# Kernel tuning notes

Hardware: AMD Instinct MI355X
Metric: run time of the kernel (lower is better)

## Reference

```python
import jax, jax.numpy as jnp
import numpy as np

B = 65536
STATE_DIM = 96
ACTION_DIM = 32
IN_FEATURES = STATE_DIM + ACTION_DIM  # 128
HIDDEN = 256
NUM_HEADS = 200
OUT_FEATURES = 1


def setup_inputs() -> dict:
    key = jax.random.key(0)
    ks = jax.random.split(key, 9)
    state = jax.random.normal(ks[0], (B, STATE_DIM), dtype=jnp.float32)
    action = jax.random.normal(ks[1], (B, ACTION_DIM), dtype=jnp.float32)
    alphas = jax.random.uniform(ks[2], (NUM_HEADS,), dtype=jnp.float32)
    W1 = jax.random.normal(ks[3], (HIDDEN, IN_FEATURES), dtype=jnp.float32) * 0.05
    b1 = jax.random.normal(ks[4], (HIDDEN,), dtype=jnp.float32) * 0.05
    W2 = jax.random.normal(ks[5], (HIDDEN, HIDDEN), dtype=jnp.float32) * 0.05
    b2 = jax.random.normal(ks[6], (HIDDEN,), dtype=jnp.float32) * 0.05
    # stacked head params: heads[h] is Linear(256 -> out_features)
    Wh = jax.random.normal(ks[7], (NUM_HEADS, OUT_FEATURES, HIDDEN), dtype=jnp.float32) * 0.05
    bh = jax.random.normal(ks[8], (NUM_HEADS, OUT_FEATURES), dtype=jnp.float32) * 0.05
    return {"state": state, "action": action, "alphas": alphas,
            "W1": W1, "b1": b1, "W2": W2, "b2": b2, "Wh": Wh, "bh": bh}


def reference(state, action, alphas, W1, b1, W2, b2, Wh, bh):
    x = jnp.concatenate([state, action], axis=1)          # [B, 128]
    x = jax.nn.relu(x @ W1.T + b1)                         # [B, 256]
    x = jax.nn.relu(x @ W2.T + b2)                         # [B, 256]
    # sum_h alpha_h * (x @ Wh[h].T + bh[h])  ==  x @ (sum_h alpha_h Wh[h]).T + sum_h alpha_h bh[h]
    Wc = jnp.einsum('h,hod->od', alphas, Wh)               # [out, 256]
    bc = jnp.einsum('h,ho->o', alphas, bh)                 # [out]
    return x @ Wc.T + bc                                   # [B, out]
```

## Files before the change

### kernel.cpp

```cpp
#include <hip/hip_runtime.h>
#include <hip/hip_bf16.h>


#define B_TOTAL 65536
#define SDIM 96
#define ADIM 32
#define IN_F 128
#define HID 256
#define NHEADS 200
#define BM 64
#define NTILES 4
#define XS_PITCH 132
#define H1_PITCH 260

typedef __bf16 bf16;
typedef __attribute__((ext_vector_type(4))) __bf16 bf16x4;
typedef __attribute__((ext_vector_type(8))) __bf16 bf16x8;
typedef __attribute__((ext_vector_type(4))) float f32x4;

__global__ __launch_bounds__(512, 2) void critic_kernel(
        const float* __restrict__ state, const float* __restrict__ action,
        const float* __restrict__ alphas,
        const float* __restrict__ W1, const float* __restrict__ b1,
        const float* __restrict__ W2, const float* __restrict__ b2,
        const float* __restrict__ Wh, const float* __restrict__ bh,
        float* __restrict__ out) {

    __shared__ bf16 xs[BM * XS_PITCH];
    __shared__ bf16 h1s[BM * H1_PITCH];
    __shared__ float sPart[8][BM];
    __shared__ float wcs[2][HID];
    __shared__ float bcs;

    const int tid  = threadIdx.x;
    const int wave = tid >> 6;
    const int lane = tid & 63;
    const int q    = lane >> 4;
    const int ln   = lane & 15;
    const int colw = wave * 32;
    const int brow0 = blockIdx.x * (BM * NTILES);

    float4 px[2][2];
    #pragma unroll
    for (int i = 0; i < 2; ++i) {
        const int c  = tid + i * 512;
        const int r  = c >> 4;
        const int c8 = c & 15;
        const float* src = (c8 < 12) ? (state  + (size_t)(brow0 + r) * SDIM + c8 * 8)
                                     : (action + (size_t)(brow0 + r) * ADIM + (c8 - 12) * 8);
        px[i][0] = ((const float4*)src)[0];
        px[i][1] = ((const float4*)src)[1];
    }

    {
        const int j    = tid & 255;
        const int half = tid >> 8;
        const int h0   = half * 100;
        float a = 0.f;
        #pragma unroll 10
        for (int hh = 0; hh < 100; ++hh) {
            const int h = h0 + hh;
            a += alphas[h] * Wh[(size_t)h * HID + j];
        }
        wcs[half][j] = a;
    }
    if (tid < 64) {
        float p = 0.f;
        for (int h = tid; h < NHEADS; h += 64) p += alphas[h] * bh[h];
        #pragma unroll
        for (int s = 1; s < 64; s <<= 1) p += __shfl_xor(p, s, 64);
        if (tid == 0) bcs = p;
    }

    bf16x8 w1f[4][2];
    #pragma unroll
    for (int ks = 0; ks < 4; ++ks)
        #pragma unroll
        for (int nt = 0; nt < 2; ++nt) {
            const float* p = &W1[(size_t)(colw + nt * 16 + ln) * IN_F + ks * 32 + q * 8];
            float4 lo = ((const float4*)p)[0];
            float4 hi = ((const float4*)p)[1];
            w1f[ks][nt] = (bf16x8){(bf16)lo.x, (bf16)lo.y, (bf16)lo.z, (bf16)lo.w,
                                   (bf16)hi.x, (bf16)hi.y, (bf16)hi.z, (bf16)hi.w};
        }

    bf16x8 w2f[8][2];
    #pragma unroll
    for (int ks = 0; ks < 8; ++ks)
        #pragma unroll
        for (int nt = 0; nt < 2; ++nt) {
            const float* p = &W2[(size_t)(colw + nt * 16 + ln) * HID + ks * 32 + q * 8];
            float4 lo = ((const float4*)p)[0];
            float4 hi = ((const float4*)p)[1];
            w2f[ks][nt] = (bf16x8){(bf16)lo.x, (bf16)lo.y, (bf16)lo.z, (bf16)lo.w,
                                   (bf16)hi.x, (bf16)hi.y, (bf16)hi.z, (bf16)hi.w};
        }

    f32x4 b1v[2], b2v[2], wcv[2];
    #pragma unroll
    for (int nt = 0; nt < 2; ++nt) {
        const int n4 = colw + nt * 16 + q * 4;
        b1v[nt] = *(const f32x4*)&b1[n4];
        b2v[nt] = *(const f32x4*)&b2[n4];
    }
    __syncthreads();
    #pragma unroll
    for (int nt = 0; nt < 2; ++nt) {
        const int n4 = colw + nt * 16 + q * 4;
        const f32x4 w0 = *(const f32x4*)&wcs[0][n4];
        const f32x4 w1v = *(const f32x4*)&wcs[1][n4];
        #pragma unroll
        for (int r = 0; r < 4; ++r) wcv[nt][r] = w0[r] + w1v[r];
    }
    const float bc = bcs;

    for (int t = 0; t < NTILES; ++t) {
        const int row0 = brow0 + t * BM;

        #pragma unroll
        for (int i = 0; i < 2; ++i) {
            const int c  = tid + i * 512;
            const int r  = c >> 4;
            const int c8 = c & 15;
            bf16x8 v = (bf16x8){(bf16)px[i][0].x, (bf16)px[i][0].y, (bf16)px[i][0].z, (bf16)px[i][0].w,
                                (bf16)px[i][1].x, (bf16)px[i][1].y, (bf16)px[i][1].z, (bf16)px[i][1].w};
            *(bf16x8*)&xs[r * XS_PITCH + c8 * 8] = v;
        }
        __syncthreads();

        if (t + 1 < NTILES) {
            const int nrow0 = row0 + BM;
            #pragma unroll
            for (int i = 0; i < 2; ++i) {
                const int c  = tid + i * 512;
                const int r  = c >> 4;
                const int c8 = c & 15;
                const float* src = (c8 < 12) ? (state  + (size_t)(nrow0 + r) * SDIM + c8 * 8)
                                             : (action + (size_t)(nrow0 + r) * ADIM + (c8 - 12) * 8);
                px[i][0] = ((const float4*)src)[0];
                px[i][1] = ((const float4*)src)[1];
            }
        }

        f32x4 acc[4][2];
        #pragma unroll
        for (int mt = 0; mt < 4; ++mt)
            #pragma unroll
            for (int nt = 0; nt < 2; ++nt)
                acc[mt][nt] = (f32x4){0.f, 0.f, 0.f, 0.f};

        #pragma unroll
        for (int ks = 0; ks < 4; ++ks) {
            const int k0 = ks * 32 + q * 8;
            bf16x8 bfr[4];
            #pragma unroll
            for (int mt = 0; mt < 4; ++mt)
                bfr[mt] = *(const bf16x8*)&xs[(mt * 16 + ln) * XS_PITCH + k0];
            #pragma unroll
            for (int mt = 0; mt < 4; ++mt)
                #pragma unroll
                for (int nt = 0; nt < 2; ++nt)
                    acc[mt][nt] = __builtin_amdgcn_mfma_f32_16x16x32_bf16(w1f[ks][nt], bfr[mt], acc[mt][nt], 0, 0, 0);
        }

        #pragma unroll
        for (int nt = 0; nt < 2; ++nt) {
            #pragma unroll
            for (int mt = 0; mt < 4; ++mt) {
                bf16x4 v4;
                #pragma unroll
                for (int r = 0; r < 4; ++r) {
                    float v = acc[mt][nt][r] + b1v[nt][r];
                    v = v > 0.f ? v : 0.f;
                    v4[r] = (bf16)v;
                }
                *(bf16x4*)&h1s[(mt * 16 + ln) * H1_PITCH + colw + nt * 16 + q * 4] = v4;
            }
        }
        __syncthreads();

        #pragma unroll
        for (int mt = 0; mt < 4; ++mt)
            #pragma unroll
            for (int nt = 0; nt < 2; ++nt)
                acc[mt][nt] = (f32x4){0.f, 0.f, 0.f, 0.f};

        #pragma unroll
        for (int ks = 0; ks < 8; ++ks) {
            const int k0 = ks * 32 + q * 8;
            bf16x8 bfr[4];
            #pragma unroll
            for (int mt = 0; mt < 4; ++mt)
                bfr[mt] = *(const bf16x8*)&h1s[(mt * 16 + ln) * H1_PITCH + k0];
            #pragma unroll
            for (int mt = 0; mt < 4; ++mt)
                #pragma unroll
                for (int nt = 0; nt < 2; ++nt)
                    acc[mt][nt] = __builtin_amdgcn_mfma_f32_16x16x32_bf16(w2f[ks][nt], bfr[mt], acc[mt][nt], 0, 0, 0);
        }

        float partial[4];
        #pragma unroll
        for (int mt = 0; mt < 4; ++mt) {
            float p = 0.f;
            #pragma unroll
            for (int nt = 0; nt < 2; ++nt)
                #pragma unroll
                for (int r = 0; r < 4; ++r) {
                    float v = acc[mt][nt][r] + b2v[nt][r];
                    v = v > 0.f ? v : 0.f;
                    p += v * wcv[nt][r];
                }
            partial[mt] = p;
        }
        #pragma unroll
        for (int mt = 0; mt < 4; ++mt) {
            partial[mt] += __shfl_xor(partial[mt], 16, 64);
            partial[mt] += __shfl_xor(partial[mt], 32, 64);
        }
        if (q == 0) {
            #pragma unroll
            for (int mt = 0; mt < 4; ++mt)
                sPart[wave][mt * 16 + ln] = partial[mt];
        }
        __syncthreads();

        if (tid < BM) {
            float v = bc;
            #pragma unroll
            for (int w = 0; w < 8; ++w) v += sPart[w][tid];
            out[row0 + tid] = v;
        }
    }
}

extern "C" void kernel_launch(void* const* d_in, const int* in_sizes, int n_in,
                              void* d_out, int out_size, void* d_ws, size_t ws_size,
                              hipStream_t stream) {
    const float* state  = (const float*)d_in[0];
    const float* action = (const float*)d_in[1];
    const float* alphas = (const float*)d_in[2];
    const float* W1     = (const float*)d_in[3];
    const float* b1     = (const float*)d_in[4];
    const float* W2     = (const float*)d_in[5];
    const float* b2     = (const float*)d_in[6];
    const float* Wh     = (const float*)d_in[7];
    const float* bh     = (const float*)d_in[8];
    float* out = (float*)d_out;

    (void)d_ws; (void)ws_size;

    critic_kernel<<<B_TOTAL / (BM * NTILES), 512, 0, stream>>>(
        state, action, alphas, W1, b1, W2, b2, Wh, bh, out);
}
```

Baseline: 110.7 us.

## Double-buffer input tile in LDS and prefetch two tiles ahead

After: 111.3 us. No clear change (+0.6%).

```diff
diff --git a/kernel.cpp b/kernel.cpp
--- a/kernel.cpp
+++ b/kernel.cpp
@@ -18,7 +18,7 @@
 typedef __attribute__((ext_vector_type(8))) __bf16 bf16x8;
 typedef __attribute__((ext_vector_type(4))) float f32x4;
 
-__global__ __launch_bounds__(512, 2) void critic_kernel(
+__global__ __launch_bounds__(512, 1) void critic_kernel(
         const float* __restrict__ state, const float* __restrict__ action,
         const float* __restrict__ alphas,
         const float* __restrict__ W1, const float* __restrict__ b1,
@@ -26,7 +26,7 @@
         const float* __restrict__ Wh, const float* __restrict__ bh,
         float* __restrict__ out) {
 
-    __shared__ bf16 xs[BM * XS_PITCH];
+    __shared__ bf16 xs[2][BM * XS_PITCH];
     __shared__ bf16 h1s[BM * H1_PITCH];
     __shared__ float sPart[8][BM];
     __shared__ float wcs[2][HID];
@@ -40,16 +40,20 @@
     const int colw = wave * 32;
     const int brow0 = blockIdx.x * (BM * NTILES);
 
+    const int c0_  = tid;
+    const int r0_  = c0_ >> 4,  cc0 = c0_ & 15;
+    const int r1_  = (c0_ + 512) >> 4, cc1 = (c0_ + 512) & 15;
+
     float4 px[2][2];
-    #pragma unroll
-    for (int i = 0; i < 2; ++i) {
-        const int c  = tid + i * 512;
-        const int r  = c >> 4;
-        const int c8 = c & 15;
-        const float* src = (c8 < 12) ? (state  + (size_t)(brow0 + r) * SDIM + c8 * 8)
-                                     : (action + (size_t)(brow0 + r) * ADIM + (c8 - 12) * 8);
-        px[i][0] = ((const float4*)src)[0];
-        px[i][1] = ((const float4*)src)[1];
+    {
+        const float* s0 = (cc0 < 12) ? (state  + (size_t)(brow0 + r0_) * SDIM + cc0 * 8)
+                                     : (action + (size_t)(brow0 + r0_) * ADIM + (cc0 - 12) * 8);
+        px[0][0] = ((const float4*)s0)[0];
+        px[0][1] = ((const float4*)s0)[1];
+        const float* s1 = (cc1 < 12) ? (state  + (size_t)(brow0 + r1_) * SDIM + cc1 * 8)
+                                     : (action + (size_t)(brow0 + r1_) * ADIM + (cc1 - 12) * 8);
+        px[1][0] = ((const float4*)s1)[0];
+        px[1][1] = ((const float4*)s1)[1];
     }
 
     {
@@ -103,11 +107,32 @@
         b1v[nt] = *(const f32x4*)&b1[n4];
         b2v[nt] = *(const f32x4*)&b2[n4];
     }
+
+    {
+        bf16x8 v0 = (bf16x8){(bf16)px[0][0].x, (bf16)px[0][0].y, (bf16)px[0][0].z, (bf16)px[0][0].w,
+                             (bf16)px[0][1].x, (bf16)px[0][1].y, (bf16)px[0][1].z, (bf16)px[0][1].w};
+        *(bf16x8*)&xs[0][r0_ * XS_PITCH + cc0 * 8] = v0;
+        bf16x8 v1 = (bf16x8){(bf16)px[1][0].x, (bf16)px[1][0].y, (bf16)px[1][0].z, (bf16)px[1][0].w,
+                             (bf16)px[1][1].x, (bf16)px[1][1].y, (bf16)px[1][1].z, (bf16)px[1][1].w};
+        *(bf16x8*)&xs[0][r1_ * XS_PITCH + cc1 * 8] = v1;
+    }
+    {
+        const int nrow0 = brow0 + BM;
+        const float* s0 = (cc0 < 12) ? (state  + (size_t)(nrow0 + r0_) * SDIM + cc0 * 8)
+                                     : (action + (size_t)(nrow0 + r0_) * ADIM + (cc0 - 12) * 8);
+        px[0][0] = ((const float4*)s0)[0];
+        px[0][1] = ((const float4*)s0)[1];
+        const float* s1 = (cc1 < 12) ? (state  + (size_t)(nrow0 + r1_) * SDIM + cc1 * 8)
+                                     : (action + (size_t)(nrow0 + r1_) * ADIM + (cc1 - 12) * 8);
+        px[1][0] = ((const float4*)s1)[0];
+        px[1][1] = ((const float4*)s1)[1];
+    }
     __syncthreads();
+
     #pragma unroll
     for (int nt = 0; nt < 2; ++nt) {
         const int n4 = colw + nt * 16 + q * 4;
-        const f32x4 w0 = *(const f32x4*)&wcs[0][n4];
+        const f32x4 w0  = *(const f32x4*)&wcs[0][n4];
         const f32x4 w1v = *(const f32x4*)&wcs[1][n4];
         #pragma unroll
         for (int r = 0; r < 4; ++r) wcv[nt][r] = w0[r] + w1v[r];
@@ -116,31 +141,8 @@
 
     for (int t = 0; t < NTILES; ++t) {
         const int row0 = brow0 + t * BM;
-
-        #pragma unroll
-        for (int i = 0; i < 2; ++i) {
-            const int c  = tid + i * 512;
-            const int r  = c >> 4;
-            const int c8 = c & 15;
-            bf16x8 v = (bf16x8){(bf16)px[i][0].x, (bf16)px[i][0].y, (bf16)px[i][0].z, (bf16)px[i][0].w,
-                                (bf16)px[i][1].x, (bf16)px[i][1].y, (bf16)px[i][1].z, (bf16)px[i][1].w};
-            *(bf16x8*)&xs[r * XS_PITCH + c8 * 8] = v;
-        }
-        __syncthreads();
-
-        if (t + 1 < NTILES) {
-            const int nrow0 = row0 + BM;
-            #pragma unroll
-            for (int i = 0; i < 2; ++i) {
-                const int c  = tid + i * 512;
-                const int r  = c >> 4;
-                const int c8 = c & 15;
-                const float* src = (c8 < 12) ? (state  + (size_t)(nrow0 + r) * SDIM + c8 * 8)
-                                             : (action + (size_t)(nrow0 + r) * ADIM + (c8 - 12) * 8);
-                px[i][0] = ((const float4*)src)[0];
-                px[i][1] = ((const float4*)src)[1];
-            }
-        }
+        const int cur  = t & 1;
+        const int nxt  = cur ^ 1;
 
         f32x4 acc[4][2];
         #pragma unroll
@@ -155,12 +157,32 @@
             bf16x8 bfr[4];
             #pragma unroll
             for (int mt = 0; mt < 4; ++mt)
-                bfr[mt] = *(const bf16x8*)&xs[(mt * 16 + ln) * XS_PITCH + k0];
+                bfr[mt] = *(const bf16x8*)&xs[cur][(mt * 16 + ln) * XS_PITCH + k0];
             #pragma unroll
             for (int mt = 0; mt < 4; ++mt)
                 #pragma unroll
                 for (int nt = 0; nt < 2; ++nt)
                     acc[mt][nt] = __builtin_amdgcn_mfma_f32_16x16x32_bf16(w1f[ks][nt], bfr[mt], acc[mt][nt], 0, 0, 0);
+        }
+
+        if (t + 1 < NTILES) {
+            bf16x8 v0 = (bf16x8){(bf16)px[0][0].x, (bf16)px[0][0].y, (bf16)px[0][0].z, (bf16)px[0][0].w,
+                                 (bf16)px[0][1].x, (bf16)px[0][1].y, (bf16)px[0][1].z, (bf16)px[0][1].w};
+            *(bf16x8*)&xs[nxt][r0_ * XS_PITCH + cc0 * 8] = v0;
+            bf16x8 v1 = (bf16x8){(bf16)px[1][0].x, (bf16)px[1][0].y, (bf16)px[1][0].z, (bf16)px[1][0].w,
+                                 (bf16)px[1][1].x, (bf16)px[1][1].y, (bf16)px[1][1].z, (bf16)px[1][1].w};
+            *(bf16x8*)&xs[nxt][r1_ * XS_PITCH + cc1 * 8] = v1;
+        }
+        if (t + 2 < NTILES) {
+            const int nrow0 = row0 + 2 * BM;
+            const float* s0 = (cc0 < 12) ? (state  + (size_t)(nrow0 + r0_) * SDIM + cc0 * 8)
+                                         : (action + (size_t)(nrow0 + r0_) * ADIM + (cc0 - 12) * 8);
+            px[0][0] = ((const float4*)s0)[0];
+            px[0][1] = ((const float4*)s0)[1];
+            const float* s1 = (cc1 < 12) ? (state  + (size_t)(nrow0 + r1_) * SDIM + cc1 * 8)
+                                         : (action + (size_t)(nrow0 + r1_) * ADIM + (cc1 - 12) * 8);
+            px[1][0] = ((const float4*)s1)[0];
+            px[1][1] = ((const float4*)s1)[1];
         }
 
         #pragma unroll
```
